# Kernel tuning notes

Measured on AMD Instinct MI355X. Metric: run time of the kernel, lower is better.

## Reference

```python
import jax, jax.numpy as jnp
import numpy as np

N_NODES = 100000
N_EDGES = 1600000
D = 64


def _sage_conv(x, src, dst, W_l, W_r, b):
    # PyG SAGEConv (aggr='mean'): out_i = W_l @ mean_{j in N(i)} x_j + W_r @ x_i + b
    n = x.shape[0]
    msgs = x[src]  # [E, D] gather of source-node features
    agg = jax.ops.segment_sum(msgs, dst, num_segments=n)  # [N, D]
    cnt = jax.ops.segment_sum(jnp.ones((src.shape[0],), x.dtype), dst, num_segments=n)
    mean = agg / jnp.maximum(cnt, 1.0)[:, None]
    return mean @ W_l.T + x @ W_r.T + b


def setup_inputs() -> dict:
    key = jax.random.key(0)
    ks = jax.random.split(key, 8)
    s = 1.0 / np.sqrt(D)
    x = jax.random.normal(ks[0], (N_NODES, D), dtype=jnp.float32)
    edge_index = jax.random.randint(ks[1], (2, N_EDGES), 0, N_NODES, dtype=jnp.int64)
    return {
        "x": x,
        "edge_index": edge_index,
        "W1_l": jax.random.normal(ks[2], (D, D), dtype=jnp.float32) * s,
        "W1_r": jax.random.normal(ks[3], (D, D), dtype=jnp.float32) * s,
        "b1": jnp.zeros((D,), dtype=jnp.float32),
        "W2_l": jax.random.normal(ks[4], (D, D), dtype=jnp.float32) * s,
        "W2_r": jax.random.normal(ks[5], (D, D), dtype=jnp.float32) * s,
        "b2": jnp.zeros((D,), dtype=jnp.float32),
    }


def reference(x, edge_index, W1_l, W1_r, b1, W2_l, W2_r, b2):
    src, dst = edge_index[0], edge_index[1]
    h = _sage_conv(x, src, dst, W1_l, W1_r, b1)
    h = jax.nn.relu(h)
    out = _sage_conv(h, src, dst, W2_l, W2_r, b2)
    return out
```

## Files before the change

kernel.cpp:

```cpp
#include <hip/hip_runtime.h>

#define D 64
#define BSHIFT 8
#define BNODES (1 << BSHIFT)
#define NBK_MAX 1024
#define CAPSH 13

typedef __attribute__((ext_vector_type(8))) short bf16x8;
typedef __attribute__((ext_vector_type(4))) float f32x4;

__device__ __forceinline__ unsigned int f2bf_rne(float f) {
    unsigned int b = __float_as_uint(f);
    return (b + 0x7fffu + ((b >> 16) & 1u)) >> 16;
}
__device__ __forceinline__ unsigned int pack_bf(float lo, float hi) {
    return f2bf_rne(lo) | (f2bf_rne(hi) << 16);
}
__device__ __forceinline__ float bflo(unsigned int u) { return __uint_as_float(u << 16); }
__device__ __forceinline__ float bfhi(unsigned int u) { return __uint_as_float(u & 0xffff0000u); }

__global__ void cast_kernel(const float4* __restrict__ xin, uint2* __restrict__ xb, int n4,
                            int* __restrict__ cnt, int nz) {
    int gid = blockIdx.x * blockDim.x + threadIdx.x;
    if (gid < nz) cnt[gid] = 0;
    int stride = gridDim.x * blockDim.x;
    for (int i = gid; i < n4; i += stride) {
        float4 v = xin[i];
        uint2 o;
        o.x = pack_bf(v.x, v.y);
        o.y = pack_bf(v.z, v.w);
        xb[i] = o;
    }
}

__global__ __launch_bounds__(256) void binscatter_kernel(
    const int* __restrict__ src, const int* __restrict__ dst,
    int* __restrict__ cnt, unsigned int* __restrict__ pairs,
    int E, int NBK, int CE) {
    __shared__ int lh[NBK_MAX];
    __shared__ int lbase[NBK_MAX];
    for (int k = threadIdx.x; k < NBK; k += 256) lh[k] = 0;
    __syncthreads();
    int b = blockIdx.x;
    int beg = b * CE, end = min(beg + CE, E);
    for (int e = beg + threadIdx.x; e < end; e += 256)
        atomicAdd(&lh[dst[e] >> BSHIFT], 1);
    __syncthreads();
    for (int k = threadIdx.x; k < NBK; k += 256) {
        int c = lh[k];
        if (c) lbase[k] = (k << CAPSH) + atomicAdd(&cnt[k], c);
        lh[k] = 0;
    }
    __syncthreads();
    for (int e = beg + threadIdx.x; e < end; e += 256) {
        int d = dst[e];
        int k = d >> BSHIFT;
        int r = atomicAdd(&lh[k], 1);
        pairs[lbase[k] + r] = (unsigned int)src[e] | ((unsigned int)(d & (BNODES - 1)) << 17);
    }
}

__global__ __launch_bounds__(256) void csr_build_kernel(
    const unsigned int* __restrict__ pairs, const int* __restrict__ cnt,
    int2* __restrict__ rowpair, int* __restrict__ csr, int N, int NBK) {
    __shared__ int lcnt[BNODES];
    __shared__ int s[256];
    int k = blockIdx.x;
    int tid = threadIdx.x;
    int node0 = k << BSHIFT;
    int nnodes = min(BNODES, N - node0);
    int rbeg = k << CAPSH, rend = rbeg + cnt[k];

    for (int j = tid; j < BNODES; j += 256) lcnt[j] = 0;
    __syncthreads();
    for (int i = rbeg + tid; i < rend; i += 256)
        atomicAdd(&lcnt[pairs[i] >> 17], 1);
    __syncthreads();
    int v0 = lcnt[tid];
    s[tid] = v0;
    __syncthreads();
    for (int off = 1; off < 256; off <<= 1) {
        int t = (tid >= off) ? s[tid - off] : 0;
        __syncthreads();
        s[tid] += t;
        __syncthreads();
    }
    int ebase = s[tid] - v0;
    __syncthreads();
    if (tid < nnodes) {
        int p = rbeg + ebase;
        rowpair[node0 + tid] = make_int2(p, p + v0);
        lcnt[tid] = p;
    }
    __syncthreads();
    for (int i = rbeg + tid; i < rend; i += 256) {
        unsigned int rec = pairs[i];
        int j = rec >> 17;
        int pos = atomicAdd(&lcnt[j], 1);
        csr[pos] = (int)(rec & 0x1FFFFu);
    }
}

__global__ __launch_bounds__(256) void fused_layer_kernel(
    const unsigned int* __restrict__ xin, const int2* __restrict__ rowpair,
    const int* __restrict__ csr,
    const float* __restrict__ Wl, const float* __restrict__ Wr,
    const float* __restrict__ bias,
    float* __restrict__ outf, unsigned int* __restrict__ outb, int N, int relu) {
    __shared__ uint4 smean[64][8];

    int tid = threadIdx.x;
    int wave = tid >> 6;
    int lane = tid & 63;
    int node0 = blockIdx.x * 64;

    int q  = lane >> 3;
    int fl = lane & 7;
    for (int o = 0; o < 2; ++o) {
        int nl = (wave << 4) + (o << 3) + q;
        int node = node0 + nl;
        bool valid = node < N;
        int beg = 0, end = 0;
        if (valid) { int2 be = rowpair[node]; beg = be.x; end = be.y; }
        float s0 = 0.f, s1 = 0.f, s2 = 0.f, s3 = 0.f;
        float s4 = 0.f, s5 = 0.f, s6 = 0.f, s7 = 0.f;
        int j = beg;
        for (; j + 4 <= end; j += 4) {
            int i0 = csr[j], i1 = csr[j + 1], i2 = csr[j + 2], i3 = csr[j + 3];
            uint4 u0 = *(const uint4*)(xin + i0 * 32 + fl * 4);
            uint4 u1 = *(const uint4*)(xin + i1 * 32 + fl * 4);
            uint4 u2 = *(const uint4*)(xin + i2 * 32 + fl * 4);
            uint4 u3 = *(const uint4*)(xin + i3 * 32 + fl * 4);
            s0 += bflo(u0.x) + bflo(u1.x) + bflo(u2.x) + bflo(u3.x);
            s1 += bfhi(u0.x) + bfhi(u1.x) + bfhi(u2.x) + bfhi(u3.x);
            s2 += bflo(u0.y) + bflo(u1.y) + bflo(u2.y) + bflo(u3.y);
            s3 += bfhi(u0.y) + bfhi(u1.y) + bfhi(u2.y) + bfhi(u3.y);
            s4 += bflo(u0.z) + bflo(u1.z) + bflo(u2.z) + bflo(u3.z);
            s5 += bfhi(u0.z) + bfhi(u1.z) + bfhi(u2.z) + bfhi(u3.z);
            s6 += bflo(u0.w) + bflo(u1.w) + bflo(u2.w) + bflo(u3.w);
            s7 += bfhi(u0.w) + bfhi(u1.w) + bfhi(u2.w) + bfhi(u3.w);
        }
        for (; j < end; ++j) {
            uint4 u = *(const uint4*)(xin + csr[j] * 32 + fl * 4);
            s0 += bflo(u.x); s1 += bfhi(u.x);
            s2 += bflo(u.y); s3 += bfhi(u.y);
            s4 += bflo(u.z); s5 += bfhi(u.z);
            s6 += bflo(u.w); s7 += bfhi(u.w);
        }
        float inv = valid ? 1.0f / fmaxf((float)(end - beg), 1.0f) : 0.f;
        uint4 ov;
        ov.x = pack_bf(s0 * inv, s1 * inv);
        ov.y = pack_bf(s2 * inv, s3 * inv);
        ov.z = pack_bf(s4 * inv, s5 * inv);
        ov.w = pack_bf(s6 * inv, s7 * inv);
        smean[nl][fl ^ (nl & 7)] = ov;
    }

    int lm   = lane & 15;
    int quad = lane >> 4;
    int f_a  = (wave << 4) + lm;
    bf16x8 wh[4], wlo[4];
#pragma unroll
    for (int s = 0; s < 4; ++s) {
        int k8 = s * 32 + quad * 8;
        const float* Wsrc = (k8 < 64) ? Wl : Wr;
        const float* p = Wsrc + f_a * 64 + (k8 & 63);
        float4 w0 = *(const float4*)p;
        float4 w1 = *(const float4*)(p + 4);
        float w[8] = {w0.x, w0.y, w0.z, w0.w, w1.x, w1.y, w1.z, w1.w};
        bf16x8 h, l;
#pragma unroll
        for (int jj = 0; jj < 8; ++jj) {
            unsigned int hb = f2bf_rne(w[jj]);
            float hf = __uint_as_float(hb << 16);
            unsigned int lb = f2bf_rne(w[jj] - hf);
            h[jj] = (short)hb;
            l[jj] = (short)lb;
        }
        wh[s] = h;
        wlo[s] = l;
    }

    __syncthreads();

    f32x4 acc[4];
#pragma unroll
    for (int nt = 0; nt < 4; ++nt) acc[nt] = (f32x4){0.f, 0.f, 0.f, 0.f};

#pragma unroll
    for (int nt = 0; nt < 4; ++nt) {
        int nl = nt * 16 + lm;
        int node = node0 + nl;
        bool v = node < N;
        const unsigned int* xrow = xin + (long long)node * 32;
#pragma unroll
        for (int s = 0; s < 2; ++s) {
            union { uint4 u4; bf16x8 v8; } cv;
            cv.u4 = smean[nl][(s * 4 + quad) ^ (lm & 7)];
            acc[nt] = __builtin_amdgcn_mfma_f32_16x16x32_bf16(wh[s],  cv.v8, acc[nt], 0, 0, 0);
            acc[nt] = __builtin_amdgcn_mfma_f32_16x16x32_bf16(wlo[s], cv.v8, acc[nt], 0, 0, 0);
        }
#pragma unroll
        for (int s = 2; s < 4; ++s) {
            uint4 u = make_uint4(0u, 0u, 0u, 0u);
            if (v) u = *(const uint4*)(xrow + ((s & 1) << 4) + (quad << 2));
            union { uint4 u4; bf16x8 v8; } cv;
            cv.u4 = u;
            acc[nt] = __builtin_amdgcn_mfma_f32_16x16x32_bf16(wh[s],  cv.v8, acc[nt], 0, 0, 0);
            acc[nt] = __builtin_amdgcn_mfma_f32_16x16x32_bf16(wlo[s], cv.v8, acc[nt], 0, 0, 0);
        }
    }

    int fb = (wave << 4) + quad * 4;
    float4 bv = *(const float4*)(bias + fb);
#pragma unroll
    for (int nt = 0; nt < 4; ++nt) {
        int node = node0 + nt * 16 + lm;
        if (node >= N) continue;
        float r0 = acc[nt][0] + bv.x;
        float r1 = acc[nt][1] + bv.y;
        float r2 = acc[nt][2] + bv.z;
        float r3 = acc[nt][3] + bv.w;
        if (relu) {
            r0 = fmaxf(r0, 0.f); r1 = fmaxf(r1, 0.f);
            r2 = fmaxf(r2, 0.f); r3 = fmaxf(r3, 0.f);
        }
        if (outf) *(float4*)(outf + (long long)node * D + fb) = make_float4(r0, r1, r2, r3);
        if (outb) *(uint2*)(outb + (long long)node * 32 + (fb >> 1)) =
                      make_uint2(pack_bf(r0, r1), pack_bf(r2, r3));
    }
}

extern "C" void kernel_launch(void* const* d_in, const int* in_sizes, int n_in,
                              void* d_out, int out_size, void* d_ws, size_t ws_size,
                              hipStream_t stream) {
    const float* x   = (const float*)d_in[0];
    const int* ei    = (const int*)d_in[1];
    const float* W1l = (const float*)d_in[2];
    const float* W1r = (const float*)d_in[3];
    const float* b1  = (const float*)d_in[4];
    const float* W2l = (const float*)d_in[5];
    const float* W2r = (const float*)d_in[6];
    const float* b2  = (const float*)d_in[7];

    const int E = in_sizes[1] / 2;
    const int N = in_sizes[0] / D;
    const int* src  = ei;
    const int* dstp = ei + E;
    const int NBK = (N + BNODES - 1) >> BSHIFT;
    const int G1 = 512;
    const int CE = (E + G1 - 1) / G1;

    char* ws = (char*)d_ws;
    size_t off = 0;
    auto alloc = [&](size_t bytes) { void* p = ws + off; off = (off + bytes + 255) & ~(size_t)255; return p; };
    int* cnt            = (int*)alloc((size_t)NBK * 4);
    int2* rowpair       = (int2*)alloc((size_t)N * 8);
    unsigned int* pairs = (unsigned int*)alloc(((size_t)NBK << CAPSH) * 4);
    int* csr            = (int*)alloc(((size_t)NBK << CAPSH) * 4);
    unsigned int* xb    = (unsigned int*)alloc((size_t)N * 32 * 4);
    unsigned int* hb    = (unsigned int*)alloc((size_t)N * 32 * 4);

    float* out = (float*)d_out;

    cast_kernel<<<2048, 256, 0, stream>>>((const float4*)x, (uint2*)xb, N * 16, cnt, NBK);

    binscatter_kernel<<<G1, 256, 0, stream>>>(src, dstp, cnt, pairs, E, NBK, CE);
    csr_build_kernel<<<NBK, 256, 0, stream>>>(pairs, cnt, rowpair, csr, N, NBK);

    const int linGrid = (N + 63) / 64;

    fused_layer_kernel<<<linGrid, 256, 0, stream>>>(xb, rowpair, csr, W1l, W1r, b1,
                                                    nullptr, hb, N, 1);
    fused_layer_kernel<<<linGrid, 256, 0, stream>>>(hb, rowpair, csr, W2l, W2r, b2,
                                                    out, nullptr, N, 0);
}
```

Before: 238.9 us.

## Pad CSR rows to 4-aligned, stage pairs in LDS, resize binscatter launch

Each node's CSR row start is padded to a multiple of four, so the gather loop can fetch four neighbor indices with one aligned int4 load instead of four scalar loads. The CSR build kernel copies each bucket's pairs into shared memory once, so the second pass reads LDS rather than global memory again. The binscatter kernel now uses 128 blocks of 512 threads to cut per-bucket global atomics, at the risk of leaving many CUs idle. Padding uses more of each bucket's fixed capacity, and the 32KB LDS buffer may lower csr_build occupancy.

```diff
diff --git a/kernel.cpp b/kernel.cpp
--- a/kernel.cpp
+++ b/kernel.cpp
@@ -3,7 +3,7 @@
 #define D 64
 #define BSHIFT 8
 #define BNODES (1 << BSHIFT)
-#define NBK_MAX 1024
+#define NBK_MAX 512
 #define CAPSH 13
 
 typedef __attribute__((ext_vector_type(8))) short bf16x8;
@@ -33,26 +33,26 @@
     }
 }
 
-__global__ __launch_bounds__(256) void binscatter_kernel(
+__global__ __launch_bounds__(512) void binscatter_kernel(
     const int* __restrict__ src, const int* __restrict__ dst,
     int* __restrict__ cnt, unsigned int* __restrict__ pairs,
     int E, int NBK, int CE) {
     __shared__ int lh[NBK_MAX];
     __shared__ int lbase[NBK_MAX];
-    for (int k = threadIdx.x; k < NBK; k += 256) lh[k] = 0;
+    for (int k = threadIdx.x; k < NBK; k += 512) lh[k] = 0;
     __syncthreads();
     int b = blockIdx.x;
     int beg = b * CE, end = min(beg + CE, E);
-    for (int e = beg + threadIdx.x; e < end; e += 256)
+    for (int e = beg + threadIdx.x; e < end; e += 512)
         atomicAdd(&lh[dst[e] >> BSHIFT], 1);
     __syncthreads();
-    for (int k = threadIdx.x; k < NBK; k += 256) {
+    for (int k = threadIdx.x; k < NBK; k += 512) {
         int c = lh[k];
         if (c) lbase[k] = (k << CAPSH) + atomicAdd(&cnt[k], c);
         lh[k] = 0;
     }
     __syncthreads();
-    for (int e = beg + threadIdx.x; e < end; e += 256) {
+    for (int e = beg + threadIdx.x; e < end; e += 512) {
         int d = dst[e];
         int k = d >> BSHIFT;
         int r = atomicAdd(&lh[k], 1);
@@ -63,21 +63,27 @@
 __global__ __launch_bounds__(256) void csr_build_kernel(
     const unsigned int* __restrict__ pairs, const int* __restrict__ cnt,
     int2* __restrict__ rowpair, int* __restrict__ csr, int N, int NBK) {
+    __shared__ unsigned int spr[1 << CAPSH];
     __shared__ int lcnt[BNODES];
     __shared__ int s[256];
     int k = blockIdx.x;
     int tid = threadIdx.x;
     int node0 = k << BSHIFT;
     int nnodes = min(BNODES, N - node0);
-    int rbeg = k << CAPSH, rend = rbeg + cnt[k];
+    int rbeg = k << CAPSH;
+    int cntk = cnt[k];
 
     for (int j = tid; j < BNODES; j += 256) lcnt[j] = 0;
     __syncthreads();
-    for (int i = rbeg + tid; i < rend; i += 256)
-        atomicAdd(&lcnt[pairs[i] >> 17], 1);
+    for (int i = tid; i < cntk; i += 256) {
+        unsigned int rec = pairs[rbeg + i];
+        spr[i] = rec;
+        atomicAdd(&lcnt[rec >> 17], 1);
+    }
     __syncthreads();
     int v0 = lcnt[tid];
-    s[tid] = v0;
+    int ps = (v0 + 3) & ~3;
+    s[tid] = ps;
     __syncthreads();
     for (int off = 1; off < 256; off <<= 1) {
         int t = (tid >= off) ? s[tid - off] : 0;
@@ -85,16 +91,13 @@
         s[tid] += t;
         __syncthreads();
     }
-    int ebase = s[tid] - v0;
-    __syncthreads();
-    if (tid < nnodes) {
-        int p = rbeg + ebase;
-        rowpair[node0 + tid] = make_int2(p, p + v0);
-        lcnt[tid] = p;
-    }
-    __syncthreads();
-    for (int i = rbeg + tid; i < rend; i += 256) {
-        unsigned int rec = pairs[i];
+    int ebase = s[tid] - ps;
+    int p = rbeg + ebase;
+    if (tid < nnodes) rowpair[node0 + tid] = make_int2(p, p + v0);
+    lcnt[tid] = p;
+    __syncthreads();
+    for (int i = tid; i < cntk; i += 256) {
+        unsigned int rec = spr[i];
         int j = rec >> 17;
         int pos = atomicAdd(&lcnt[j], 1);
         csr[pos] = (int)(rec & 0x1FFFFu);
@@ -126,11 +129,11 @@
         float s4 = 0.f, s5 = 0.f, s6 = 0.f, s7 = 0.f;
         int j = beg;
         for (; j + 4 <= end; j += 4) {
-            int i0 = csr[j], i1 = csr[j + 1], i2 = csr[j + 2], i3 = csr[j + 3];
-            uint4 u0 = *(const uint4*)(xin + i0 * 32 + fl * 4);
-            uint4 u1 = *(const uint4*)(xin + i1 * 32 + fl * 4);
-            uint4 u2 = *(const uint4*)(xin + i2 * 32 + fl * 4);
-            uint4 u3 = *(const uint4*)(xin + i3 * 32 + fl * 4);
+            int4 iv = *(const int4*)(csr + j);
+            uint4 u0 = *(const uint4*)(xin + iv.x * 32 + fl * 4);
+            uint4 u1 = *(const uint4*)(xin + iv.y * 32 + fl * 4);
+            uint4 u2 = *(const uint4*)(xin + iv.z * 32 + fl * 4);
+            uint4 u3 = *(const uint4*)(xin + iv.w * 32 + fl * 4);
             s0 += bflo(u0.x) + bflo(u1.x) + bflo(u2.x) + bflo(u3.x);
             s1 += bfhi(u0.x) + bfhi(u1.x) + bfhi(u2.x) + bfhi(u3.x);
             s2 += bflo(u0.y) + bflo(u1.y) + bflo(u2.y) + bflo(u3.y);
@@ -248,7 +251,7 @@
     const int* src  = ei;
     const int* dstp = ei + E;
     const int NBK = (N + BNODES - 1) >> BSHIFT;
-    const int G1 = 512;
+    const int G1 = 128;
     const int CE = (E + G1 - 1) / G1;
 
     char* ws = (char*)d_ws;
@@ -265,7 +268,7 @@
 
     cast_kernel<<<2048, 256, 0, stream>>>((const float4*)x, (uint2*)xb, N * 16, cnt, NBK);
 
-    binscatter_kernel<<<G1, 256, 0, stream>>>(src, dstp, cnt, pairs, E, NBK, CE);
+    binscatter_kernel<<<G1, 512, 0, stream>>>(src, dstp, cnt, pairs, E, NBK, CE);
     csr_build_kernel<<<NBK, 256, 0, stream>>>(pairs, cnt, rowpair, csr, N, NBK);
 
     const int linGrid = (N + 63) / 64;
```

Result: faster. 232.8 us (-2.5%).
